# Kernel tuning notes

Measured on AMD Instinct MI355X. Metric: run time of the kernel, lower is better.

Reference implementation:

```python
import jax, jax.numpy as jnp
import numpy as np
import math

SEQ_LEN = 2048
D_MODEL = 512
HEADS = 8
HEAD_DIM = D_MODEL // HEADS
BATCH = 4


def setup_inputs() -> dict:
    key = jax.random.key(0)
    ks = jax.random.split(key, 12)
    s = 0.02
    return {
        "query": jax.random.normal(ks[0], (BATCH, SEQ_LEN, D_MODEL), dtype=jnp.float32),
        "Wq": jax.random.normal(ks[1], (D_MODEL, D_MODEL), dtype=jnp.float32) * s,
        "bq": jnp.zeros((D_MODEL,), dtype=jnp.float32),
        "Wk": jax.random.normal(ks[2], (D_MODEL, D_MODEL), dtype=jnp.float32) * s,
        "bk": jnp.zeros((D_MODEL,), dtype=jnp.float32),
        "Wv": jax.random.normal(ks[3], (D_MODEL, D_MODEL), dtype=jnp.float32) * s,
        "bv": jnp.zeros((D_MODEL,), dtype=jnp.float32),
        "Wp": jax.random.normal(ks[4], (D_MODEL, D_MODEL), dtype=jnp.float32) * s,
        "bp": jnp.zeros((D_MODEL,), dtype=jnp.float32),
        "logit_scale": jnp.full((HEADS, 1, 1), math.log(10.0), dtype=jnp.float32),
        "rpe": jax.random.normal(ks[5], (2 * SEQ_LEN - 1, HEADS), dtype=jnp.float32) * s,
    }


def reference(query, Wq, bq, Wk, bk, Wv, bv, Wp, bp, logit_scale, rpe):
    N, S, D = query.shape
    H = HEADS

    def split_heads(x):
        # reshape(N, S, head_dim, H) then permute(0, 3, 1, 2) -> (N, H, S, head_dim)
        return x.reshape(N, S, D // H, H).transpose(0, 3, 1, 2)

    q = split_heads(query @ Wq.T + bq)
    k = split_heads(query @ Wk.T + bk)  # key defaults to query
    v = split_heads(query @ Wv.T + bv)  # value defaults to key

    attn = jnp.einsum("bhqd,bhkd->bhqk", q, k) / math.sqrt(D)
    scale = jnp.exp(jnp.minimum(logit_scale, math.log(1.0 / 0.01)))  # (H,1,1)
    attn = attn * scale[None]

    # relative position bias: idx[i,j] = i - j + S - 1
    idx = jnp.arange(S)[:, None] - jnp.arange(S)[None, :] + (S - 1)  # (S,S)
    bias = jax.nn.sigmoid(rpe[idx].transpose(2, 0, 1))  # (H,S,S)
    attn = attn + bias[None]

    attn = jax.nn.softmax(attn, axis=-1)
    out = jnp.einsum("bhqk,bhkd->bhqd", attn, v)
    out = out.transpose(0, 2, 1, 3).reshape(N, S, D)
    return out @ Wp.T + bp
```

## Files before the change

### kernel.cpp

```cpp
#include <hip/hip_runtime.h>
#include <math.h>

#define N_B 4
#define SEQ 2048
#define DM  512
#define H_N 8
#define DH  64

typedef unsigned short ushort_t;
typedef __attribute__((ext_vector_type(8))) short short8_t;
typedef __attribute__((ext_vector_type(4))) float float4_t;

#define LOG2E 1.4426950408889634074f

__device__ __forceinline__ ushort_t f2bf(float f) {
    unsigned int x = __float_as_uint(f);
    unsigned int lsb = (x >> 16) & 1u;
    x += 0x7fffu + lsb;
    return (ushort_t)(x >> 16);
}
__device__ __forceinline__ unsigned int cvtpk_bf16(float a, float b) {
    unsigned int r;
    asm("v_cvt_pk_bf16_f32 %0, %1, %2" : "=v"(r) : "v"(a), "v"(b));
    return r;
}
__device__ __forceinline__ float fexp2(float x) {
#if __has_builtin(__builtin_amdgcn_exp2f)
    return __builtin_amdgcn_exp2f(x);
#else
    return exp2f(x);
#endif
}
__device__ __forceinline__ void gload_lds16(const ushort_t* g, ushort_t* l) {
    __builtin_amdgcn_global_load_lds((const __attribute__((address_space(1))) void*)g,
                                     (__attribute__((address_space(3))) void*)l,
                                     16, 0, 0);
}

#define Q4 1048576
#define W4 65536
#define RELN 4095
#define GTABN (H_N * RELN)
__global__ __launch_bounds__(256)
void prep(const float* __restrict__ query,
          const float* __restrict__ Wq, const float* __restrict__ Wk,
          const float* __restrict__ Wv, const float* __restrict__ Wp,
          const float* __restrict__ bq, const float* __restrict__ bk,
          const float* __restrict__ bv, const float* __restrict__ bp,
          const float* __restrict__ rpe,
          ushort_t* __restrict__ q16, ushort_t* __restrict__ w16,
          float* __restrict__ bcat, float* __restrict__ gtab)
{
    int i = blockIdx.x * 256 + threadIdx.x;
    if (i < Q4) {
        float4 x = ((const float4*)query)[i];
        uint2 p;
        p.x = cvtpk_bf16(x.x, x.y);
        p.y = cvtpk_bf16(x.z, x.w);
        ((uint2*)q16)[i] = p;
    } else if (i < Q4 + 4 * W4) {
        int wi = i - Q4;
        int w = wi >> 16;
        const float* W = (w == 0) ? Wq : (w == 1) ? Wk : (w == 2) ? Wv : Wp;
        int gwi = wi & (W4 - 1);
        int c = gwi >> 7;
        int g = gwi & 127;
        float4 x = ((const float4*)W)[gwi];
        uint2 p;
        p.x = cvtpk_bf16(x.x, x.y);
        p.y = cvtpk_bf16(x.z, x.w);
        int c2 = (w < 3) ? (((c & 7) << 6) | (c >> 3)) : c;
        ((uint2*)w16)[w * W4 + c2 * 128 + g] = p;
    } else if (i < Q4 + 4 * W4 + 2048) {
        int bi = i - (Q4 + 4 * W4);
        int seg = bi >> 9;
        int c = bi & 511;
        const float* B = (seg == 0) ? bq : (seg == 1) ? bk : (seg == 2) ? bv : bp;
        int c2 = (seg < 3) ? (((c & 7) << 6) | (c >> 3)) : c;
        bcat[seg * 512 + c2] = B[c];
    } else {
        int gi = i - (Q4 + 4 * W4 + 2048);
        if (gi < GTABN) {
            int h = gi / RELN;
            int rel = gi - h * RELN;
            float4 v;
            #pragma unroll
            for (int c = 0; c < 4; c++) {
                int rr = rel - c;
                if (rr < 0) rr = 0;
                float x = rpe[rr * H_N + h];
                ((float*)&v)[c] = LOG2E / (1.0f + __expf(-x));
            }
            ((float4*)gtab)[gi] = v;
        }
    }
}

template<int MODE>
__global__ __launch_bounds__(256)
void mgemm(const ushort_t* __restrict__ A, const ushort_t* __restrict__ B,
           const float* __restrict__ bias,
           ushort_t* __restrict__ q_o, ushort_t* __restrict__ k_o,
           ushort_t* __restrict__ vt_o, float* __restrict__ p_o)
{
    __shared__ __align__(16) union SM {
        struct { ushort_t A[128][64]; ushort_t B[128][64]; } ab;
        ushort_t C[128][128];
    } sm;
    ushort_t (&As)[128][64] = sm.ab.A;
    ushort_t (&Bs)[128][64] = sm.ab.B;

    const int t     = threadIdx.x;
    const int wid   = t >> 6;
    const int lane  = t & 63;
    const int lan16 = lane & 15;
    const int quad  = lane >> 4;
    const int wm    = (wid & 1) * 64;
    const int wn    = (wid >> 1) * 64;

    const int col0 = blockIdx.x * 128;
    const int row0 = blockIdx.y * 128;

    const int srow = lane >> 3;
    const int gchk = (lane & 7) ^ ((lane >> 3) & 7);
    const ushort_t* gA = A + (size_t)(row0 + wid * 8 + srow) * DM + gchk * 8;
    const ushort_t* gB = B + (size_t)(col0 + wid * 8 + srow) * DM + gchk * 8;

    float4_t acc[4][4];
    #pragma unroll
    for (int i = 0; i < 4; i++)
        #pragma unroll
        for (int j = 0; j < 4; j++) acc[i][j] = (float4_t){0.f, 0.f, 0.f, 0.f};

    const int sw = lan16 & 7;

    for (int k0 = 0; k0 < DM; k0 += 64) {
        __syncthreads();
        #pragma unroll
        for (int j = 0; j < 4; j++) {
            gload_lds16(gA + k0 + (size_t)j * 32 * DM, &As[j * 32 + wid * 8][0]);
            gload_lds16(gB + k0 + (size_t)j * 32 * DM, &Bs[j * 32 + wid * 8][0]);
        }
        asm volatile("s_waitcnt vmcnt(0)" ::: "memory");
        __syncthreads();

        #pragma unroll
        for (int kk = 0; kk < 2; kk++) {
            short8_t af[4], bf[4];
            #pragma unroll
            for (int i = 0; i < 4; i++) {
                af[i] = *(const short8_t*)&As[wm + i * 16 + lan16][((kk * 4 + quad) ^ sw) * 8];
                bf[i] = *(const short8_t*)&Bs[wn + i * 16 + lan16][((kk * 4 + quad) ^ sw) * 8];
            }
            #pragma unroll
            for (int i = 0; i < 4; i++)
                #pragma unroll
                for (int j = 0; j < 4; j++)
                    acc[i][j] = __builtin_amdgcn_mfma_f32_16x16x32_bf16(af[i], bf[j], acc[i][j], 0, 0, 0);
        }
    }

    if (MODE == 1) {
        #pragma unroll
        for (int j = 0; j < 4; j++) {
            int col = col0 + wn + j * 16 + lan16;
            float bv = bias[col];
            #pragma unroll
            for (int i = 0; i < 4; i++) {
                #pragma unroll
                for (int reg = 0; reg < 4; reg++) {
                    int row = row0 + wm + i * 16 + quad * 4 + reg;
                    p_o[(size_t)row * DM + col] = acc[i][j][reg] + bv;
                }
            }
        }
        return;
    }

    const int w = col0 >> 9;
    __syncthreads();

    if (w < 2) {
        #pragma unroll
        for (int j = 0; j < 4; j++) {
            float bv = bias[col0 + wn + j * 16 + lan16];
            #pragma unroll
            for (int i = 0; i < 4; i++)
                #pragma unroll
                for (int reg = 0; reg < 4; reg++)
                    sm.C[wm + i * 16 + quad * 4 + reg][wn + j * 16 + lan16] =
                        f2bf(acc[i][j][reg] + bv);
        }
    } else {
        #pragma unroll
        for (int j = 0; j < 4; j++) {
            float bv = bias[col0 + wn + j * 16 + lan16];
            #pragma unroll
            for (int i = 0; i < 4; i++) {
                uint2 pw;
                pw.x = cvtpk_bf16(acc[i][j][0] + bv, acc[i][j][1] + bv);
                pw.y = cvtpk_bf16(acc[i][j][2] + bv, acc[i][j][3] + bv);
                *(uint2*)&sm.C[wn + j * 16 + lan16][wm + i * 16 + quad * 4] = pw;
            }
        }
    }
    __syncthreads();

    const int n   = row0 >> 11;
    const int s0  = row0 & 2047;
    const int hh0 = (col0 & 511) >> 6;

    if (w < 2) {
        ushort_t* dst = (w == 0) ? q_o : k_o;
        #pragma unroll
        for (int it = 0; it < 8; it++) {
            int ch  = it * 256 + t;
            int s   = ch >> 4;
            int c16 = ch & 15;
            int head = hh0 + (c16 >> 3);
            int dq   = (c16 & 7) * 8;
            size_t a = (((size_t)(n * H_N + head)) * SEQ + (s0 + s)) * DH + dq;
            *(uint4*)(dst + a) = *(const uint4*)&sm.C[s][c16 * 8];
        }
    } else {
        #pragma unroll
        for (int it = 0; it < 8; it++) {
            int ch = it * 256 + t;
            int r  = ch >> 4;
            int sg = ch & 15;
            int head = hh0 + (r >> 6);
            int dh   = r & 63;
            size_t a = (((size_t)(n * H_N + head)) * DH + dh) * SEQ + s0 + sg * 8;
            *(uint4*)(vt_o + a) = *(const uint4*)&sm.C[r][sg * 8];
        }
    }
}

__global__ __launch_bounds__(256)
void attn_k(const ushort_t* __restrict__ qw, const ushort_t* __restrict__ kw,
            const ushort_t* __restrict__ vt, const float* __restrict__ lsc,
            const float* __restrict__ gtab, ushort_t* __restrict__ ctx)
{
    __shared__ __align__(16) ushort_t K_s[2][64][72];
    __shared__ __align__(16) ushort_t VT_s[2][64][72];
    __shared__ __align__(16) unsigned int Pp[4][2][16][36];

    const int t     = threadIdx.x;
    const int wid   = t >> 6;
    const int lane  = t & 63;
    const int lan16 = lane & 15;
    const int quad  = lane >> 4;

    const int h  = blockIdx.x;
    const int qt = blockIdx.y;
    const int n  = blockIdx.z;
    const int q0 = qt * 128;

    const size_t headoff = ((size_t)(n * H_N + h)) * SEQ * DH;
    const ushort_t* qh  = qw + headoff;
    const ushort_t* kh  = kw + headoff;
    const ushort_t* vth = vt + headoff;

    float ls = lsc[h];
    const float lm = 4.60517018598809136804f;
    if (ls > lm) ls = lm;
    const float scale2 = __expf(ls) * 0.04419417382415921757f * LOG2E;

    const int qrow0 = q0 + wid * 32 + lan16;
    const float4* gt = (const float4*)gtab + (size_t)h * RELN + (qrow0 + 2047 - quad * 4);

    short8_t qb[2][2];
    #pragma unroll
    for (int qf = 0; qf < 2; qf++) {
        const ushort_t* src = qh + (size_t)(qrow0 + qf * 16) * DH + quad * 8;
        qb[qf][0] = *(const short8_t*)(src);
        qb[qf][1] = *(const short8_t*)(src + 32);
    }

    float l_run[2] = {0.f, 0.f};
    float4_t o[4][2];
    #pragma unroll
    for (int ds = 0; ds < 4; ds++)
        #pragma unroll
        for (int qf = 0; qf < 2; qf++) o[ds][qf] = (float4_t){0.f, 0.f, 0.f, 0.f};

    const int srow = t >> 2;
    const int sc   = (t & 3) * 16;
    const ushort_t* kbase = kh + (size_t)srow * DH + sc;
    const ushort_t* vbase = vth + (size_t)srow * SEQ + sc;

    float4 b4E[2][4];
    {
        uint4 k0r = *(const uint4*)(kbase);
        uint4 k1r = *(const uint4*)(kbase + 8);
        uint4 v0r = *(const uint4*)(vbase);
        uint4 v1r = *(const uint4*)(vbase + 8);
        #pragma unroll
        for (int qf = 0; qf < 2; qf++)
            #pragma unroll
            for (int sub = 0; sub < 4; sub++) b4E[qf][sub] = gt[(qf - sub) * 16];
        *(uint4*)&K_s[0][srow][sc]      = k0r;
        *(uint4*)&K_s[0][srow][sc + 8]  = k1r;
        *(uint4*)&VT_s[0][srow][sc]     = v0r;
        *(uint4*)&VT_s[0][srow][sc + 8] = v1r;
    }
    __syncthreads();

#define COMPUTE(B, B4)                                                               \
  {                                                                                  \
    float4_t st[4][2];                                                               \
    _Pragma("unroll")                                                                \
    for (int sub = 0; sub < 4; sub++) {                                              \
        const ushort_t* kp_ = &K_s[B][sub * 16 + lan16][quad * 8];                   \
        short8_t ka0 = *(const short8_t*)(kp_);                                      \
        short8_t ka1 = *(const short8_t*)(kp_ + 32);                                 \
        _Pragma("unroll")                                                            \
        for (int qf = 0; qf < 2; qf++) {                                             \
            float4_t a = (float4_t){0.f, 0.f, 0.f, 0.f};                             \
            a = __builtin_amdgcn_mfma_f32_16x16x32_bf16(ka0, qb[qf][0], a, 0, 0, 0); \
            a = __builtin_amdgcn_mfma_f32_16x16x32_bf16(ka1, qb[qf][1], a, 0, 0, 0); \
            st[sub][qf] = a;                                                         \
        }                                                                            \
    }                                                                                \
    _Pragma("unroll")                                                                \
    for (int qf = 0; qf < 2; qf++) {                                                 \
        float ps = 0.f;                                                              \
        _Pragma("unroll")                                                            \
        for (int sub = 0; sub < 4; sub++) {                                          \
            float e0 = fexp2(st[sub][qf][0] * scale2 + B4[qf][sub].x);               \
            float e1 = fexp2(st[sub][qf][1] * scale2 + B4[qf][sub].y);               \
            float e2 = fexp2(st[sub][qf][2] * scale2 + B4[qf][sub].z);               \
            float e3 = fexp2(st[sub][qf][3] * scale2 + B4[qf][sub].w);               \
            ps += (e0 + e1) + (e2 + e3);                                             \
            uint2 pw;                                                                \
            pw.x = cvtpk_bf16(e0, e1);                                               \
            pw.y = cvtpk_bf16(e2, e3);                                               \
            *(uint2*)&Pp[wid][qf][lan16][sub * 8 + quad * 2] = pw;                   \
        }                                                                            \
        l_run[qf] += ps;                                                             \
    }                                                                                \
    asm volatile("s_waitcnt lgkmcnt(0)" ::: "memory");                               \
    _Pragma("unroll")                                                                \
    for (int ks = 0; ks < 2; ks++) {                                                 \
        short8_t pb[2];                                                              \
        _Pragma("unroll")                                                            \
        for (int qf = 0; qf < 2; qf++)                                               \
            pb[qf] = *(const short8_t*)&Pp[wid][qf][lan16][ks * 16 + quad * 4];      \
        _Pragma("unroll")                                                            \
        for (int ds = 0; ds < 4; ds++) {                                             \
            short8_t va = *(const short8_t*)&VT_s[B][ds * 16 + lan16][ks * 32 + quad * 8]; \
            _Pragma("unroll")                                                        \
            for (int qf = 0; qf < 2; qf++)                                           \
                o[ds][qf] = __builtin_amdgcn_mfma_f32_16x16x32_bf16(va, pb[qf], o[ds][qf], 0, 0, 0); \
        }                                                                            \
    }                                                                                \
  }

    #pragma unroll 1
    for (int it = 0; it < 16; it++) {
        const int j0a = it * 128;

        {
            uint4 kr0 = *(const uint4*)(kbase + (size_t)(j0a + 64) * DH);
            uint4 kr1 = *(const uint4*)(kbase + (size_t)(j0a + 64) * DH + 8);
            uint4 vr0 = *(const uint4*)(vbase + (j0a + 64));
            uint4 vr1 = *(const uint4*)(vbase + (j0a + 64) + 8);
            float4 b4O[2][4];
            {
                const float4* gtp = gt - (j0a + 64);
                #pragma unroll
                for (int qf = 0; qf < 2; qf++)
                    #pragma unroll
                    for (int sub = 0; sub < 4; sub++) b4O[qf][sub] = gtp[(qf - sub) * 16];
            }

            COMPUTE(0, b4E);

            *(uint4*)&K_s[1][srow][sc]      = kr0;
            *(uint4*)&K_s[1][srow][sc + 8]  = kr1;
            *(uint4*)&VT_s[1][srow][sc]     = vr0;
            *(uint4*)&VT_s[1][srow][sc + 8] = vr1;
            __syncthreads();

            if (it < 15) {
                uint4 ke0 = *(const uint4*)(kbase + (size_t)(j0a + 128) * DH);
                uint4 ke1 = *(const uint4*)(kbase + (size_t)(j0a + 128) * DH + 8);
                uint4 ve0 = *(const uint4*)(vbase + (j0a + 128));
                uint4 ve1 = *(const uint4*)(vbase + (j0a + 128) + 8);
                {
                    const float4* gtp = gt - (j0a + 128);
                    #pragma unroll
                    for (int qf = 0; qf < 2; qf++)
                        #pragma unroll
                        for (int sub = 0; sub < 4; sub++) b4E[qf][sub] = gtp[(qf - sub) * 16];
                }

                COMPUTE(1, b4O);

                *(uint4*)&K_s[0][srow][sc]      = ke0;
                *(uint4*)&K_s[0][srow][sc + 8]  = ke1;
                *(uint4*)&VT_s[0][srow][sc]     = ve0;
                *(uint4*)&VT_s[0][srow][sc + 8] = ve1;
                __syncthreads();
            } else {
                COMPUTE(1, b4O);
            }
        }
    }
#undef COMPUTE

    #pragma unroll
    for (int qf = 0; qf < 2; qf++) {
        float l = l_run[qf];
        l += __shfl_xor(l, 16);
        l += __shfl_xor(l, 32);
        float inv = 1.0f / l;
        int row = qrow0 + qf * 16;
        size_t base = ((size_t)n * SEQ + row) * DM + h * DH;
        #pragma unroll
        for (int ds = 0; ds < 4; ds++) {
            uint2 p;
            p.x = cvtpk_bf16(o[ds][qf][0] * inv, o[ds][qf][1] * inv);
            p.y = cvtpk_bf16(o[ds][qf][2] * inv, o[ds][qf][3] * inv);
            *(uint2*)(ctx + base + ds * 16 + quad * 4) = p;
        }
    }
}

extern "C" void kernel_launch(void* const* d_in, const int* in_sizes, int n_in,
                              void* d_out, int out_size, void* d_ws, size_t ws_size,
                              hipStream_t stream) {
    const float* query = (const float*)d_in[0];
    const float* Wq  = (const float*)d_in[1];
    const float* bq  = (const float*)d_in[2];
    const float* Wk  = (const float*)d_in[3];
    const float* bk  = (const float*)d_in[4];
    const float* Wv  = (const float*)d_in[5];
    const float* bv  = (const float*)d_in[6];
    const float* Wp  = (const float*)d_in[7];
    const float* bp  = (const float*)d_in[8];
    const float* lsc = (const float*)d_in[9];
    const float* rpe = (const float*)d_in[10];

    const size_t QEL = (size_t)N_B * SEQ * DM;
    const size_t WEL = (size_t)DM * DM;
    char* ws = (char*)d_ws;
    ushort_t* q16  = (ushort_t*)(ws);
    ushort_t* w16  = q16 + QEL;
    float*    bcat = (float*)(w16 + 4 * WEL);
    float*    gtab = bcat + 2048;
    ushort_t* qb   = (ushort_t*)(gtab + 4 * GTABN);
    ushort_t* kb   = qb + QEL;
    ushort_t* vtb  = kb + QEL;
    ushort_t* ctx  = vtb + QEL;

    const int PREPN = Q4 + 4 * W4 + 2048 + GTABN;
    prep<<<(PREPN + 255) / 256, 256, 0, stream>>>(
        query, Wq, Wk, Wv, Wp, bq, bk, bv, bp, rpe, q16, w16, bcat, gtab);

    dim3 g1(1536 / 128, (N_B * SEQ) / 128);
    mgemm<0><<<g1, 256, 0, stream>>>(q16, w16, bcat, qb, kb, vtb, nullptr);

    dim3 ga(H_N, SEQ / 128, N_B);
    attn_k<<<ga, 256, 0, stream>>>(qb, kb, vtb, lsc, gtab, ctx);

    dim3 g2(DM / 128, (N_B * SEQ) / 128);
    mgemm<1><<<g2, 256, 0, stream>>>(ctx, w16 + 3 * WEL, bcat + 1536,
                                     nullptr, nullptr, nullptr, (float*)d_out);
}
```

Before: 186.1 us.

## Prefetch next GEMM K-tile into registers while computing current tile

Replaces the direct global-to-LDS loads in the projection GEMM with register-staged loads. The next 64-wide K tile is fetched into registers before the MFMA loop on the current tile and written to LDS afterward. The aim is to overlap global memory latency with matrix-core work instead of stalling on vmcnt(0) each iteration. In exchange it uses extra VGPRs for staging and adds an explicit LDS store pass, and the swizzled layout in LDS now depends on the global-side chunk permutation.

```diff
diff --git a/kernel.cpp b/kernel.cpp
--- a/kernel.cpp
+++ b/kernel.cpp
@@ -30,11 +30,6 @@
 #else
     return exp2f(x);
 #endif
-}
-__device__ __forceinline__ void gload_lds16(const ushort_t* g, ushort_t* l) {
-    __builtin_amdgcn_global_load_lds((const __attribute__((address_space(1))) void*)g,
-                                     (__attribute__((address_space(3))) void*)l,
-                                     16, 0, 0);
 }
 
 #define Q4 1048576
@@ -125,6 +120,8 @@
     const int gchk = (lane & 7) ^ ((lane >> 3) & 7);
     const ushort_t* gA = A + (size_t)(row0 + wid * 8 + srow) * DM + gchk * 8;
     const ushort_t* gB = B + (size_t)(col0 + wid * 8 + srow) * DM + gchk * 8;
+    const int lrow = wid * 8 + srow;
+    const int lchk = (lane & 7) * 8;
 
     float4_t acc[4][4];
     #pragma unroll
@@ -134,15 +131,28 @@
 
     const int sw = lan16 & 7;
 
+    uint4 ra[4], rb[4];
+    #pragma unroll
+    for (int j = 0; j < 4; j++) {
+        ra[j] = *(const uint4*)(gA + (size_t)j * 32 * DM);
+        rb[j] = *(const uint4*)(gB + (size_t)j * 32 * DM);
+    }
+    #pragma unroll
+    for (int j = 0; j < 4; j++) {
+        *(uint4*)&As[j * 32 + lrow][lchk] = ra[j];
+        *(uint4*)&Bs[j * 32 + lrow][lchk] = rb[j];
+    }
+    __syncthreads();
+
     for (int k0 = 0; k0 < DM; k0 += 64) {
-        __syncthreads();
-        #pragma unroll
-        for (int j = 0; j < 4; j++) {
-            gload_lds16(gA + k0 + (size_t)j * 32 * DM, &As[j * 32 + wid * 8][0]);
-            gload_lds16(gB + k0 + (size_t)j * 32 * DM, &Bs[j * 32 + wid * 8][0]);
-        }
-        asm volatile("s_waitcnt vmcnt(0)" ::: "memory");
-        __syncthreads();
+        const bool more = (k0 + 64 < DM);
+        if (more) {
+            #pragma unroll
+            for (int j = 0; j < 4; j++) {
+                ra[j] = *(const uint4*)(gA + k0 + 64 + (size_t)j * 32 * DM);
+                rb[j] = *(const uint4*)(gB + k0 + 64 + (size_t)j * 32 * DM);
+            }
+        }
 
         #pragma unroll
         for (int kk = 0; kk < 2; kk++) {
@@ -157,6 +167,16 @@
                 #pragma unroll
                 for (int j = 0; j < 4; j++)
                     acc[i][j] = __builtin_amdgcn_mfma_f32_16x16x32_bf16(af[i], bf[j], acc[i][j], 0, 0, 0);
+        }
+
+        if (more) {
+            __syncthreads();
+            #pragma unroll
+            for (int j = 0; j < 4; j++) {
+                *(uint4*)&As[j * 32 + lrow][lchk] = ra[j];
+                *(uint4*)&Bs[j * 32 + lrow][lchk] = rb[j];
+            }
+            __syncthreads();
         }
     }
 
```

Measured after the change: 234.2 us. 1.26x slower.
